# Kernel tuning notes

Hardware: AMD Instinct MI355X
Metric: run time of the kernel (lower is better)

Reference implementation:

```python
import jax, jax.numpy as jnp
import numpy as np

SIGMA_P = 0.01  # sigma_p from __init__
T = 2_000_000   # number of time samples / PMD steps


def _pauli():
    # Pauli spin matrices used by Czegledi (2016) rotation model
    return jnp.array([[[1, 0], [0, -1]],
                      [[0, 1], [1, 0]],
                      [[0, -1j], [1j, 0]]], dtype=jnp.complex64)


def setup_inputs() -> dict:
    key = jax.random.key(0)
    k1, k2, k3, k4 = jax.random.split(key, 4)
    signal_re = jax.random.normal(k1, (T, 2), dtype=jnp.float32)
    signal_im = jax.random.normal(k2, (T, 2), dtype=jnp.float32)
    alphas = jax.random.normal(k3, (T, 3), dtype=jnp.float32)  # raw N(0,1); scaled by SIGMA_P inside reference
    # initial Jones matrix J_k1 built from a random unit 4-vector (as in __init__)
    g = jax.random.normal(k4, (4,), dtype=jnp.float32)
    a0 = g / jnp.linalg.norm(g)
    theta0 = jnp.arccos(a0[0])
    alpha = a0[1:] / jnp.sin(theta0) * theta0
    theta = jnp.linalg.norm(alpha)
    a = (alpha / theta).astype(jnp.complex64)
    J0 = (jnp.eye(2, dtype=jnp.complex64) * jnp.cos(theta)
          - 1j * jnp.einsum('a,aij->ij', a, _pauli()) * jnp.sin(theta))
    return {"signal_re": signal_re, "signal_im": signal_im, "alphas": alphas,
            "J0_re": jnp.real(J0), "J0_im": jnp.imag(J0)}


def reference(signal_re, signal_im, alphas, J0_re, J0_im):
    pauli = _pauli()
    al = alphas * SIGMA_P                      # [T,3] per-step rotation vectors
    thetas = jnp.linalg.norm(al, axis=1)       # [T]
    a = (al / thetas[:, None]).astype(jnp.complex64)   # [T,3] unit axes
    eye = jnp.eye(2, dtype=jnp.complex64)
    # per-step incremental Jones matrices: J_delta[k] = I*cos(th) - i*(a.sigma)*sin(th)
    J_delta = (eye[None, :, :] * jnp.cos(thetas)[:, None, None]
               - 1j * jnp.einsum('ka,aij->kij', a, pauli) * jnp.sin(thetas)[:, None, None])  # [T,2,2]
    # cumulative left-product: chain[k] = J_delta[k] @ ... @ J_delta[0]
    chain = jax.lax.associative_scan(lambda x, y: jnp.matmul(y, x), J_delta)  # [T,2,2]
    J0 = (J0_re + 1j * J0_im).astype(jnp.complex64)
    J_k = jnp.einsum('kij,jl->kil', chain, J0)  # [T,2,2] time-varying Jones matrices
    signal = (signal_re + 1j * signal_im).astype(jnp.complex64)  # [T,2]
    return jnp.einsum('kij,kj->ki', J_k, signal)  # [T,2] complex64
```

## Files before the change

kernel.cpp:

```cpp
#include <hip/hip_runtime.h>
#include <hip/hip_bf16.h>

#define BLK 256

__device__ __forceinline__ float4 qmul(const float4 A, const float4 B) {
    return make_float4(
        A.x*B.x - A.y*B.y - A.z*B.z - A.w*B.w,
        A.x*B.y + B.x*A.y + A.z*B.w - A.w*B.z,
        A.x*B.z + B.x*A.z + A.w*B.y - A.y*B.w,
        A.x*B.w + B.x*A.w + A.y*B.z - A.z*B.y);
}

__device__ __forceinline__ float4 qid() { return make_float4(1.f, 0.f, 0.f, 0.f); }

__device__ __forceinline__ float4 qnorm(const float4 q) {
    float n = rsqrtf(q.x*q.x + q.y*q.y + q.z*q.z + q.w*q.w);
    return make_float4(q.x*n, q.y*n, q.z*n, q.w*n);
}

__device__ __forceinline__ float4 dquat(float a0, float a1, float a2) {
    float x = a0 * 0.01f, y = a1 * 0.01f, z = a2 * 0.01f;
    float t2 = x*x + y*y + z*z;
    float c = 1.f - t2 * (0.5f - t2 * (1.f / 24.f));
    float f = 1.f - t2 * ((1.f / 6.f) - t2 * (1.f / 120.f));
    return make_float4(c, f*x, f*y, f*z);
}

__device__ __forceinline__ float4 qapply(const float4 m, float s0r, float s1r,
                                         float s0i, float s1i) {
    float w = m.x, v1 = m.y, v2 = m.z, v3 = m.w;
    return make_float4(
        w*s0r + v1*s0i - v3*s1r + v2*s1i,
        w*s0i - v1*s0r - v2*s1r - v3*s1i,
        v3*s0r + v2*s0i + w*s1r - v1*s1i,
        v3*s0i - v2*s0r + w*s1i + v1*s1r);
}

__device__ __forceinline__ float4 block_scan_incl(float4 v, float4* sh) {
    const int tid = threadIdx.x;
    sh[tid] = v;
    __syncthreads();
    #pragma unroll
    for (int d = 1; d < BLK; d <<= 1) {
        float4 other;
        bool act = tid >= d;
        if (act) other = sh[tid - d];
        __syncthreads();
        if (act) { v = qmul(v, other); sh[tid] = v; }
        __syncthreads();
    }
    return v;
}

template<int CH>
__device__ __forceinline__ float4 chunk_quats(const float* __restrict__ al,
                                              long long t, long long T,
                                              long long nchunk, float4* d, bool& full) {
    float4 q = qid();
    full = false;
    if (t >= nchunk) {
        #pragma unroll
        for (int j = 0; j < CH; ++j) d[j] = qid();
        return q;
    }
    if ((t + 1) * CH <= T) {
        full = true;
        const float4* ap = reinterpret_cast<const float4*>(al) + (size_t)t * (CH * 3 / 4);
        #pragma unroll
        for (int g = 0; g < CH / 8; ++g) {
            float4 v0 = ap[g*6+0], v1 = ap[g*6+1], v2 = ap[g*6+2];
            float4 v3 = ap[g*6+3], v4 = ap[g*6+4], v5 = ap[g*6+5];
            d[g*8+0] = dquat(v0.x, v0.y, v0.z);
            d[g*8+1] = dquat(v0.w, v1.x, v1.y);
            d[g*8+2] = dquat(v1.z, v1.w, v2.x);
            d[g*8+3] = dquat(v2.y, v2.z, v2.w);
            d[g*8+4] = dquat(v3.x, v3.y, v3.z);
            d[g*8+5] = dquat(v3.w, v4.x, v4.y);
            d[g*8+6] = dquat(v4.z, v4.w, v5.x);
            d[g*8+7] = dquat(v5.y, v5.z, v5.w);
        }
    } else {
        #pragma unroll
        for (int j = 0; j < CH; ++j) {
            long long k = t * CH + j;
            d[j] = (k < T) ? dquat(al[k*3], al[k*3+1], al[k*3+2]) : qid();
        }
    }
    #pragma unroll
    for (int j = 0; j < CH; ++j) q = qmul(d[j], q);
    return qnorm(q);
}

template<int CH>
__device__ __forceinline__ void apply_and_store(
    const float4* d, float4 run, bool full, long long t, long long T,
    const float* __restrict__ sre, const float* __restrict__ sim,
    float* __restrict__ outf) {
    if (full) {
        const float4* rp = reinterpret_cast<const float4*>(sre) + (size_t)t * (CH / 2);
        const float4* ip = reinterpret_cast<const float4*>(sim) + (size_t)t * (CH / 2);
        float4* op = reinterpret_cast<float4*>(outf) + (size_t)t * (CH / 2);
        #pragma unroll
        for (int g = 0; g < CH / 8; ++g) {
            float4 r0 = rp[g*4+0], r1 = rp[g*4+1], r2 = rp[g*4+2], r3 = rp[g*4+3];
            float4 i0 = ip[g*4+0], i1 = ip[g*4+1], i2 = ip[g*4+2], i3 = ip[g*4+3];
            float4 p0, p1;
            run = qmul(d[g*8+0], run); p0 = qapply(run, r0.x, r0.y, i0.x, i0.y);
            run = qmul(d[g*8+1], run); p1 = qapply(run, r0.z, r0.w, i0.z, i0.w);
            op[g*4+0] = make_float4(p0.x, p0.z, p1.x, p1.z);
            run = qmul(d[g*8+2], run); p0 = qapply(run, r1.x, r1.y, i1.x, i1.y);
            run = qmul(d[g*8+3], run); p1 = qapply(run, r1.z, r1.w, i1.z, i1.w);
            op[g*4+1] = make_float4(p0.x, p0.z, p1.x, p1.z);
            run = qmul(d[g*8+4], run); p0 = qapply(run, r2.x, r2.y, i2.x, i2.y);
            run = qmul(d[g*8+5], run); p1 = qapply(run, r2.z, r2.w, i2.z, i2.w);
            op[g*4+2] = make_float4(p0.x, p0.z, p1.x, p1.z);
            run = qmul(d[g*8+6], run); p0 = qapply(run, r3.x, r3.y, i3.x, i3.y);
            run = qmul(d[g*8+7], run); p1 = qapply(run, r3.z, r3.w, i3.z, i3.w);
            op[g*4+3] = make_float4(p0.x, p0.z, p1.x, p1.z);
        }
    } else {
        float2* op2 = reinterpret_cast<float2*>(outf);
        #pragma unroll
        for (int j = 0; j < CH; ++j) {
            long long k = t * CH + j;
            if (k < T) {
                run = qmul(d[j], run);
                float4 p = qapply(run, sre[k*2], sre[k*2+1], sim[k*2], sim[k*2+1]);
                op2[k] = make_float2(p.x, p.z);
            }
        }
    }
}

template<int CH>
__global__ void __launch_bounds__(BLK) pmd_k1(
    const float* __restrict__ al, float4* __restrict__ A,
    long long T, long long nchunk) {
    __shared__ float4 sh[BLK];
    const long long t = (long long)blockIdx.x * BLK + threadIdx.x;
    float4 d[CH];
    bool full;
    float4 q = chunk_quats<CH>(al, t, T, nchunk, d, full);
    float4 incl = block_scan_incl(q, sh);
    if (threadIdx.x == BLK - 1) A[blockIdx.x] = qnorm(incl);
}

template<int EPT>
__global__ void __launch_bounds__(BLK) pmd_k2(
    const float4* __restrict__ A, float4* __restrict__ EB,
    const float* __restrict__ j0re, const float* __restrict__ j0im, int nblk) {
    __shared__ float4 sh[BLK];
    const int tid = threadIdx.x;
    float4 excl[EPT];
    float4 run = qid();
    #pragma unroll
    for (int e = 0; e < EPT; ++e) {
        int idx = tid * EPT + e;
        excl[e] = run;
        if (idx < nblk) run = qmul(A[idx], run);
    }
    block_scan_incl(run, sh);
    float4 X = (tid == 0) ? qid() : sh[tid - 1];
    float4 q0 = make_float4(j0re[0], -j0im[0], -j0im[1], -j0re[1]);
    float4 base = qmul(X, q0);
    #pragma unroll
    for (int e = 0; e < EPT; ++e) {
        int idx = tid * EPT + e;
        if (idx < nblk) EB[idx] = qnorm(qmul(excl[e], base));
    }
}

template<int CH>
__global__ void __launch_bounds__(BLK) pmd_k3(
    const float* __restrict__ al, const float* __restrict__ sre,
    const float* __restrict__ sim, const float4* __restrict__ EB,
    float* __restrict__ outf, long long T, long long nchunk) {
    __shared__ float4 sh[BLK];
    const long long t = (long long)blockIdx.x * BLK + threadIdx.x;
    float4 d[CH];
    bool full;
    float4 q = chunk_quats<CH>(al, t, T, nchunk, d, full);
    block_scan_incl(q, sh);
    float4 Xv = (threadIdx.x == 0) ? qid() : sh[threadIdx.x - 1];
    if (t >= nchunk) return;
    float4 run = qmul(Xv, EB[blockIdx.x]);
    apply_and_store<CH>(d, run, full, t, T, sre, sim, outf);
}

template<int CH>
__global__ void __launch_bounds__(BLK) pmd_mono(
    const float* __restrict__ al, const float* __restrict__ sre,
    const float* __restrict__ sim, const float* __restrict__ j0re,
    const float* __restrict__ j0im, float* __restrict__ outf, long long T) {
    __shared__ float4 sh[BLK];
    __shared__ float4 sbase;
    if (threadIdx.x == 0)
        sbase = make_float4(j0re[0], -j0im[0], -j0im[1], -j0re[1]);
    __syncthreads();
    const long long nchunk = (T + CH - 1) / CH;
    for (long long c0 = 0; c0 < nchunk; c0 += BLK) {
        const long long t = c0 + threadIdx.x;
        float4 d[CH];
        bool full;
        float4 q = chunk_quats<CH>(al, t, T, nchunk, d, full);
        float4 incl = block_scan_incl(q, sh);
        float4 Xv = (threadIdx.x == 0) ? qid() : sh[threadIdx.x - 1];
        float4 base = sbase;
        __syncthreads();
        if (threadIdx.x == BLK - 1) sbase = qnorm(qmul(incl, base));
        if (t < nchunk) {
            float4 run = qmul(Xv, base);
            apply_and_store<CH>(d, run, full, t, T, sre, sim, outf);
        }
        __syncthreads();
    }
}

extern "C" void kernel_launch(void* const* d_in, const int* in_sizes, int n_in,
                              void* d_out, int out_size, void* d_ws, size_t ws_size,
                              hipStream_t stream) {
    const float* sre  = (const float*)d_in[0];
    const float* sim  = (const float*)d_in[1];
    const float* al   = (const float*)d_in[2];
    const float* j0re = (const float*)d_in[3];
    const float* j0im = (const float*)d_in[4];
    float* outf = (float*)d_out;
    long long T = (long long)in_sizes[2] / 3;
    if (T <= 0) return;

    constexpr int CH = 8;
    long long nchunk = (T + CH - 1) / CH;
    long long nblkLL = (nchunk + BLK - 1) / BLK;
    size_t need = (size_t)(2 * nblkLL) * sizeof(float4);

    if (ws_size >= need && nblkLL <= (long long)BLK * 16) {
        int nblk = (int)nblkLL;
        float4* A  = (float4*)d_ws;
        float4* EB = A + nblk;
        pmd_k1<CH><<<nblk, BLK, 0, stream>>>(al, A, T, nchunk);
        if      (nblk <= BLK)      pmd_k2<1> <<<1, BLK, 0, stream>>>(A, EB, j0re, j0im, nblk);
        else if (nblk <= 2 * BLK)  pmd_k2<2> <<<1, BLK, 0, stream>>>(A, EB, j0re, j0im, nblk);
        else if (nblk <= 4 * BLK)  pmd_k2<4> <<<1, BLK, 0, stream>>>(A, EB, j0re, j0im, nblk);
        else if (nblk <= 8 * BLK)  pmd_k2<8> <<<1, BLK, 0, stream>>>(A, EB, j0re, j0im, nblk);
        else                       pmd_k2<16><<<1, BLK, 0, stream>>>(A, EB, j0re, j0im, nblk);
        pmd_k3<CH><<<nblk, BLK, 0, stream>>>(al, sre, sim, EB, outf, T, nchunk);
    } else {
        pmd_mono<CH><<<1, BLK, 0, stream>>>(al, sre, sim, j0re, j0im, outf, T);
    }
}
```

Before: 30.62 us.

## Fuse three-kernel scan into single-pass decoupled scan with dynamic block tickets

```diff
diff --git a/kernel.cpp b/kernel.cpp
--- a/kernel.cpp
+++ b/kernel.cpp
@@ -2,6 +2,7 @@
 #include <hip/hip_bf16.h>
 
 #define BLK 256
+#define CH 8
 
 __device__ __forceinline__ float4 qmul(const float4 A, const float4 B) {
     return make_float4(
@@ -52,7 +53,17 @@
     return v;
 }
 
-template<int CH>
+__device__ __forceinline__ float4 wave_prod_desc(float4 c) {
+    #pragma unroll
+    for (int s = 1; s < 64; s <<= 1) {
+        float4 u;
+        u.x = __shfl_down(c.x, s); u.y = __shfl_down(c.y, s);
+        u.z = __shfl_down(c.z, s); u.w = __shfl_down(c.w, s);
+        c = qmul(u, c);
+    }
+    return c;
+}
+
 __device__ __forceinline__ float4 chunk_quats(const float* __restrict__ al,
                                               long long t, long long T,
                                               long long nchunk, float4* d, bool& full) {
@@ -65,20 +76,17 @@
     }
     if ((t + 1) * CH <= T) {
         full = true;
-        const float4* ap = reinterpret_cast<const float4*>(al) + (size_t)t * (CH * 3 / 4);
-        #pragma unroll
-        for (int g = 0; g < CH / 8; ++g) {
-            float4 v0 = ap[g*6+0], v1 = ap[g*6+1], v2 = ap[g*6+2];
-            float4 v3 = ap[g*6+3], v4 = ap[g*6+4], v5 = ap[g*6+5];
-            d[g*8+0] = dquat(v0.x, v0.y, v0.z);
-            d[g*8+1] = dquat(v0.w, v1.x, v1.y);
-            d[g*8+2] = dquat(v1.z, v1.w, v2.x);
-            d[g*8+3] = dquat(v2.y, v2.z, v2.w);
-            d[g*8+4] = dquat(v3.x, v3.y, v3.z);
-            d[g*8+5] = dquat(v3.w, v4.x, v4.y);
-            d[g*8+6] = dquat(v4.z, v4.w, v5.x);
-            d[g*8+7] = dquat(v5.y, v5.z, v5.w);
-        }
+        const float4* ap = reinterpret_cast<const float4*>(al) + (size_t)t * 6;
+        float4 v0 = ap[0], v1 = ap[1], v2 = ap[2];
+        float4 v3 = ap[3], v4 = ap[4], v5 = ap[5];
+        d[0] = dquat(v0.x, v0.y, v0.z);
+        d[1] = dquat(v0.w, v1.x, v1.y);
+        d[2] = dquat(v1.z, v1.w, v2.x);
+        d[3] = dquat(v2.y, v2.z, v2.w);
+        d[4] = dquat(v3.x, v3.y, v3.z);
+        d[5] = dquat(v3.w, v4.x, v4.y);
+        d[6] = dquat(v4.z, v4.w, v5.x);
+        d[7] = dquat(v5.y, v5.z, v5.w);
     } else {
         #pragma unroll
         for (int j = 0; j < CH; ++j) {
@@ -91,33 +99,29 @@
     return qnorm(q);
 }
 
-template<int CH>
 __device__ __forceinline__ void apply_and_store(
     const float4* d, float4 run, bool full, long long t, long long T,
     const float* __restrict__ sre, const float* __restrict__ sim,
     float* __restrict__ outf) {
     if (full) {
-        const float4* rp = reinterpret_cast<const float4*>(sre) + (size_t)t * (CH / 2);
-        const float4* ip = reinterpret_cast<const float4*>(sim) + (size_t)t * (CH / 2);
-        float4* op = reinterpret_cast<float4*>(outf) + (size_t)t * (CH / 2);
-        #pragma unroll
-        for (int g = 0; g < CH / 8; ++g) {
-            float4 r0 = rp[g*4+0], r1 = rp[g*4+1], r2 = rp[g*4+2], r3 = rp[g*4+3];
-            float4 i0 = ip[g*4+0], i1 = ip[g*4+1], i2 = ip[g*4+2], i3 = ip[g*4+3];
-            float4 p0, p1;
-            run = qmul(d[g*8+0], run); p0 = qapply(run, r0.x, r0.y, i0.x, i0.y);
-            run = qmul(d[g*8+1], run); p1 = qapply(run, r0.z, r0.w, i0.z, i0.w);
-            op[g*4+0] = make_float4(p0.x, p0.z, p1.x, p1.z);
-            run = qmul(d[g*8+2], run); p0 = qapply(run, r1.x, r1.y, i1.x, i1.y);
-            run = qmul(d[g*8+3], run); p1 = qapply(run, r1.z, r1.w, i1.z, i1.w);
-            op[g*4+1] = make_float4(p0.x, p0.z, p1.x, p1.z);
-            run = qmul(d[g*8+4], run); p0 = qapply(run, r2.x, r2.y, i2.x, i2.y);
-            run = qmul(d[g*8+5], run); p1 = qapply(run, r2.z, r2.w, i2.z, i2.w);
-            op[g*4+2] = make_float4(p0.x, p0.z, p1.x, p1.z);
-            run = qmul(d[g*8+6], run); p0 = qapply(run, r3.x, r3.y, i3.x, i3.y);
-            run = qmul(d[g*8+7], run); p1 = qapply(run, r3.z, r3.w, i3.z, i3.w);
-            op[g*4+3] = make_float4(p0.x, p0.z, p1.x, p1.z);
-        }
+        const float4* rp = reinterpret_cast<const float4*>(sre) + (size_t)t * 4;
+        const float4* ip = reinterpret_cast<const float4*>(sim) + (size_t)t * 4;
+        float4* op = reinterpret_cast<float4*>(outf) + (size_t)t * 4;
+        float4 r0 = rp[0], r1 = rp[1], r2 = rp[2], r3 = rp[3];
+        float4 i0 = ip[0], i1 = ip[1], i2 = ip[2], i3 = ip[3];
+        float4 p0, p1;
+        run = qmul(d[0], run); p0 = qapply(run, r0.x, r0.y, i0.x, i0.y);
+        run = qmul(d[1], run); p1 = qapply(run, r0.z, r0.w, i0.z, i0.w);
+        op[0] = make_float4(p0.x, p0.z, p1.x, p1.z);
+        run = qmul(d[2], run); p0 = qapply(run, r1.x, r1.y, i1.x, i1.y);
+        run = qmul(d[3], run); p1 = qapply(run, r1.z, r1.w, i1.z, i1.w);
+        op[1] = make_float4(p0.x, p0.z, p1.x, p1.z);
+        run = qmul(d[4], run); p0 = qapply(run, r2.x, r2.y, i2.x, i2.y);
+        run = qmul(d[5], run); p1 = qapply(run, r2.z, r2.w, i2.z, i2.w);
+        op[2] = make_float4(p0.x, p0.z, p1.x, p1.z);
+        run = qmul(d[6], run); p0 = qapply(run, r3.x, r3.y, i3.x, i3.y);
+        run = qmul(d[7], run); p1 = qapply(run, r3.z, r3.w, i3.z, i3.w);
+        op[3] = make_float4(p0.x, p0.z, p1.x, p1.z);
     } else {
         float2* op2 = reinterpret_cast<float2*>(outf);
         #pragma unroll
@@ -132,62 +136,71 @@
     }
 }
 
-template<int CH>
-__global__ void __launch_bounds__(BLK) pmd_k1(
-    const float* __restrict__ al, float4* __restrict__ A,
-    long long T, long long nchunk) {
+__global__ void __launch_bounds__(BLK) pmd_init(unsigned* __restrict__ flags, int n) {
+    int i = blockIdx.x * BLK + threadIdx.x;
+    if (i < n) flags[i] = 0u;
+}
+
+__global__ void __launch_bounds__(BLK) pmd_fused(
+    const float* __restrict__ al, const float* __restrict__ sre,
+    const float* __restrict__ sim, const float* __restrict__ j0re,
+    const float* __restrict__ j0im, float* __restrict__ outf,
+    float4* __restrict__ Aarr, unsigned* __restrict__ flags,
+    unsigned* __restrict__ ticket, long long T, long long nchunk) {
     __shared__ float4 sh[BLK];
-    const long long t = (long long)blockIdx.x * BLK + threadIdx.x;
+    __shared__ unsigned srank;
+    __shared__ float4 sexcl;
+    const int tid = threadIdx.x;
+    if (tid == 0) srank = atomicAdd(ticket, 1u);
+    __syncthreads();
+    const int rank = (int)srank;
+    const long long t = (long long)rank * BLK + tid;
+
     float4 d[CH];
     bool full;
-    float4 q = chunk_quats<CH>(al, t, T, nchunk, d, full);
-    float4 incl = block_scan_incl(q, sh);
-    if (threadIdx.x == BLK - 1) A[blockIdx.x] = qnorm(incl);
-}
-
-template<int EPT>
-__global__ void __launch_bounds__(BLK) pmd_k2(
-    const float4* __restrict__ A, float4* __restrict__ EB,
-    const float* __restrict__ j0re, const float* __restrict__ j0im, int nblk) {
-    __shared__ float4 sh[BLK];
-    const int tid = threadIdx.x;
-    float4 excl[EPT];
-    float4 run = qid();
-    #pragma unroll
-    for (int e = 0; e < EPT; ++e) {
-        int idx = tid * EPT + e;
-        excl[e] = run;
-        if (idx < nblk) run = qmul(A[idx], run);
-    }
-    block_scan_incl(run, sh);
-    float4 X = (tid == 0) ? qid() : sh[tid - 1];
-    float4 q0 = make_float4(j0re[0], -j0im[0], -j0im[1], -j0re[1]);
-    float4 base = qmul(X, q0);
-    #pragma unroll
-    for (int e = 0; e < EPT; ++e) {
-        int idx = tid * EPT + e;
-        if (idx < nblk) EB[idx] = qnorm(qmul(excl[e], base));
-    }
-}
-
-template<int CH>
-__global__ void __launch_bounds__(BLK) pmd_k3(
-    const float* __restrict__ al, const float* __restrict__ sre,
-    const float* __restrict__ sim, const float4* __restrict__ EB,
-    float* __restrict__ outf, long long T, long long nchunk) {
-    __shared__ float4 sh[BLK];
-    const long long t = (long long)blockIdx.x * BLK + threadIdx.x;
-    float4 d[CH];
-    bool full;
-    float4 q = chunk_quats<CH>(al, t, T, nchunk, d, full);
+    float4 q = chunk_quats(al, t, T, nchunk, d, full);
     block_scan_incl(q, sh);
-    float4 Xv = (threadIdx.x == 0) ? qid() : sh[threadIdx.x - 1];
-    if (t >= nchunk) return;
-    float4 run = qmul(Xv, EB[blockIdx.x]);
-    apply_and_store<CH>(d, run, full, t, T, sre, sim, outf);
-}
-
-template<int CH>
+    float4 Xv = (tid == 0) ? qid() : sh[tid - 1];
+
+    if (tid == 0) {
+        Aarr[rank] = qnorm(sh[BLK - 1]);
+        __hip_atomic_store(&flags[rank], 1u, __ATOMIC_RELEASE,
+                           __HIP_MEMORY_SCOPE_AGENT);
+        if (rank == 0) {
+            sexcl = make_float4(j0re[0], -j0im[0], -j0im[1], -j0re[1]);
+        }
+    }
+    if (rank > 0 && tid < 64) {
+        float4 excl = qid();
+        int top = rank - 1;
+        int base = (top >> 6) << 6;
+        for (;;) {
+            int j = base + tid;
+            float4 contrib = qid();
+            if (j <= top) {
+                unsigned f;
+                do {
+                    f = __hip_atomic_load(&flags[j], __ATOMIC_ACQUIRE,
+                                          __HIP_MEMORY_SCOPE_AGENT);
+                } while (f == 0u);
+                contrib = Aarr[j];
+            }
+            float4 wp = wave_prod_desc(contrib);
+            excl = qmul(excl, wp);
+            if (base == 0) break;
+            top = base - 1;
+            base -= 64;
+        }
+        if (tid == 0) {
+            float4 q0 = make_float4(j0re[0], -j0im[0], -j0im[1], -j0re[1]);
+            sexcl = qnorm(qmul(excl, q0));
+        }
+    }
+    __syncthreads();
+    float4 run = qmul(Xv, sexcl);
+    apply_and_store(d, run, full, t, T, sre, sim, outf);
+}
+
 __global__ void __launch_bounds__(BLK) pmd_mono(
     const float* __restrict__ al, const float* __restrict__ sre,
     const float* __restrict__ sim, const float* __restrict__ j0re,
@@ -202,7 +215,7 @@
         const long long t = c0 + threadIdx.x;
         float4 d[CH];
         bool full;
-        float4 q = chunk_quats<CH>(al, t, T, nchunk, d, full);
+        float4 q = chunk_quats(al, t, T, nchunk, d, full);
         float4 incl = block_scan_incl(q, sh);
         float4 Xv = (threadIdx.x == 0) ? qid() : sh[threadIdx.x - 1];
         float4 base = sbase;
@@ -210,7 +223,7 @@
         if (threadIdx.x == BLK - 1) sbase = qnorm(qmul(incl, base));
         if (t < nchunk) {
             float4 run = qmul(Xv, base);
-            apply_and_store<CH>(d, run, full, t, T, sre, sim, outf);
+            apply_and_store(d, run, full, t, T, sre, sim, outf);
         }
         __syncthreads();
     }
@@ -228,23 +241,20 @@
     long long T = (long long)in_sizes[2] / 3;
     if (T <= 0) return;
 
-    constexpr int CH = 8;
     long long nchunk = (T + CH - 1) / CH;
     long long nblkLL = (nchunk + BLK - 1) / BLK;
-    size_t need = (size_t)(2 * nblkLL) * sizeof(float4);
-
-    if (ws_size >= need && nblkLL <= (long long)BLK * 16) {
+    size_t need = (size_t)nblkLL * 16 + (size_t)(nblkLL + 1) * 4;
+
+    if (ws_size >= need && nblkLL <= (1LL << 30)) {
         int nblk = (int)nblkLL;
-        float4* A  = (float4*)d_ws;
-        float4* EB = A + nblk;
-        pmd_k1<CH><<<nblk, BLK, 0, stream>>>(al, A, T, nchunk);
-        if      (nblk <= BLK)      pmd_k2<1> <<<1, BLK, 0, stream>>>(A, EB, j0re, j0im, nblk);
-        else if (nblk <= 2 * BLK)  pmd_k2<2> <<<1, BLK, 0, stream>>>(A, EB, j0re, j0im, nblk);
-        else if (nblk <= 4 * BLK)  pmd_k2<4> <<<1, BLK, 0, stream>>>(A, EB, j0re, j0im, nblk);
-        else if (nblk <= 8 * BLK)  pmd_k2<8> <<<1, BLK, 0, stream>>>(A, EB, j0re, j0im, nblk);
-        else                       pmd_k2<16><<<1, BLK, 0, stream>>>(A, EB, j0re, j0im, nblk);
-        pmd_k3<CH><<<nblk, BLK, 0, stream>>>(al, sre, sim, EB, outf, T, nchunk);
+        float4* Aarr = (float4*)d_ws;
+        unsigned* flags = (unsigned*)((char*)d_ws + (size_t)nblk * 16);
+        unsigned* ticket = flags + nblk;
+        int ninit = nblk + 1;
+        pmd_init<<<(ninit + BLK - 1) / BLK, BLK, 0, stream>>>(flags, ninit);
+        pmd_fused<<<nblk, BLK, 0, stream>>>(al, sre, sim, j0re, j0im, outf,
+                                            Aarr, flags, ticket, T, nchunk);
     } else {
-        pmd_mono<CH><<<1, BLK, 0, stream>>>(al, sre, sim, j0re, j0im, outf, T);
-    }
-}
+        pmd_mono<<<1, BLK, 0, stream>>>(al, sre, sim, j0re, j0im, outf, T);
+    }
+}
```

After: 116.1 us. +279.3%, slower.
